# Performance work log

Measured on AMD Instinct MI355X. Metric: run time of the kernel, lower is better.

## Reference

```python
import jax, jax.numpy as jnp
import numpy as np

N = 50000
E = 800000
IN_DIM = 128
HID = 128
OUT = 4
EPS = 1e-5


def setup_inputs() -> dict:
    key = jax.random.key(0)
    ks = jax.random.split(key, 16)
    glorot = lambda k, i, o: jax.random.uniform(k, (i, o), jnp.float32, -1.0, 1.0) * jnp.sqrt(6.0 / (i + o))
    return {
        "x": jax.random.normal(ks[0], (N, IN_DIM), jnp.float32),
        "edge_index": jax.random.randint(ks[1], (2, E), 0, N, jnp.int64),
        # SAGEConv layer 0: lin_l (aggregated neighbors, with bias), lin_r (self, no bias)
        "W_l0": glorot(ks[2], IN_DIM, HID), "b_l0": jnp.zeros((HID,), jnp.float32),
        "W_r0": glorot(ks[3], IN_DIM, HID),
        # SAGEConv layer 1
        "W_l1": glorot(ks[4], HID, HID), "b_l1": jnp.zeros((HID,), jnp.float32),
        "W_r1": glorot(ks[5], HID, HID),
        # LayerNorms
        "g0": jnp.ones((HID,), jnp.float32), "beta0": jnp.zeros((HID,), jnp.float32),
        "g1": jnp.ones((HID,), jnp.float32), "beta1": jnp.zeros((HID,), jnp.float32),
        # head
        "W_h": glorot(ks[6], HID, OUT), "b_h": jnp.zeros((OUT,), jnp.float32),
    }


def _sage_conv(x, src, dst, deg_inv, W_l, b_l, W_r):
    # mean-aggregate source features at destination nodes, then project
    agg = jax.ops.segment_sum(x[src], dst, num_segments=N) * deg_inv  # [N, d]
    return agg @ W_l + b_l + x @ W_r


def _layer_norm(x, g, b):
    mu = jnp.mean(x, axis=-1, keepdims=True)
    var = jnp.mean(jnp.square(x - mu), axis=-1, keepdims=True)
    return (x - mu) * jax.lax.rsqrt(var + EPS) * g + b


def reference(x, edge_index, W_l0, b_l0, W_r0, W_l1, b_l1, W_r1, g0, beta0, g1, beta1, W_h, b_h):
    src, dst = edge_index[0], edge_index[1]
    deg = jax.ops.segment_sum(jnp.ones((E,), jnp.float32), dst, num_segments=N)
    deg_inv = (1.0 / jnp.maximum(deg, 1.0))[:, None]  # mean over empty neighborhood -> 0

    h = _sage_conv(x, src, dst, deg_inv, W_l0, b_l0, W_r0)
    h = jax.nn.relu(_layer_norm(h, g0, beta0))
    h = _sage_conv(h, src, dst, deg_inv, W_l1, b_l1, W_r1)
    h = jax.nn.relu(_layer_norm(h, g1, beta1))
    return h @ W_h + b_h  # [N, 4]
```

## Files before the change

### kernel.cpp

```cpp
#include <hip/hip_runtime.h>

#define NN 50000
#define EE 800000
#define DIM 128
#define KK 256
#define OUTD 4
#define EPSV 1e-5f
#define OTS 132
#define NB 196
#define SLOT 8192
#define ACHUNK 4096
#define NA 196

using short8v = __attribute__((ext_vector_type(8))) short;
using f32x4v  = __attribute__((ext_vector_type(4))) float;

__device__ __forceinline__ unsigned short f2bf(float f) {
    union { float f; unsigned u; } x; x.f = f;
    unsigned r = x.u + 0x7FFF + ((x.u >> 16) & 1);
    return (unsigned short)(r >> 16);
}
__device__ __forceinline__ float bf2f(unsigned short u) {
    union { unsigned u; float f; } x; x.u = ((unsigned)u) << 16;
    return x.f;
}

#define XB_BLK 6250
#define W_BLK  256
__global__ __launch_bounds__(256) void prep_kernel(
    const float* __restrict__ x, ushort* __restrict__ xb,
    const float* __restrict__ Wl0, const float* __restrict__ Wr0,
    const float* __restrict__ Wl1, const float* __restrict__ Wr1,
    ushort* __restrict__ Wt0, ushort* __restrict__ Wt1,
    int* __restrict__ bucketCursor)
{
    int b = blockIdx.x;
    if (b < XB_BLK) {
        int i = b * 256 + threadIdx.x;
        float4 v = ((const float4*)x)[i];
        ushort4 o;
        o.x = f2bf(v.x); o.y = f2bf(v.y); o.z = f2bf(v.z); o.w = f2bf(v.w);
        ((ushort4*)xb)[i] = o;
    } else if (b < XB_BLK + W_BLK) {
        int idx = (b - XB_BLK) * 256 + threadIdx.x;
        int which = idx >> 15;
        int j = (idx >> 8) & 127;
        int k = idx & 255;
        const float* Wl = which ? Wl1 : Wl0;
        const float* Wr = which ? Wr1 : Wr0;
        ushort* Wt = which ? Wt1 : Wt0;
        float v = (k < 128) ? Wl[k * DIM + j] : Wr[(k - 128) * DIM + j];
        Wt[j * KK + k] = f2bf(v);
    } else {
        if (threadIdx.x < NB) bucketCursor[threadIdx.x] = 0;
    }
}

__global__ __launch_bounds__(256) void passA_kernel(
    const int* __restrict__ src, const int* __restrict__ dst,
    int* __restrict__ bucketCursor, unsigned* __restrict__ pairs)
{
    __shared__ int hist[256];
    __shared__ int scanb[256];
    __shared__ int exStart[256];
    __shared__ int cur2[256];
    __shared__ int gBase[256];
    __shared__ unsigned stage[ACHUNK];
    int tid = threadIdx.x;
    int eBase = blockIdx.x * ACHUNK;
    int total = min(ACHUNK, EE - eBase);

    hist[tid] = 0;
    __syncthreads();

    #pragma unroll
    for (int i = 0; i < 16; i++) {
        int idx = i * 256 + tid;
        if (idx < total) {
            int d = dst[eBase + idx];
            atomicAdd(&hist[d >> 8], 1);
        }
    }
    __syncthreads();
    int cntv = hist[tid];
    scanb[tid] = cntv;
    __syncthreads();
    #pragma unroll
    for (int off = 1; off < 256; off <<= 1) {
        int add = (tid >= off) ? scanb[tid - off] : 0;
        __syncthreads();
        scanb[tid] += add;
        __syncthreads();
    }
    int ex = scanb[tid] - cntv;
    exStart[tid] = ex;
    cur2[tid] = ex;
    if (tid < NB) gBase[tid] = (cntv > 0) ? atomicAdd(&bucketCursor[tid], cntv) : 0;
    __syncthreads();

    #pragma unroll
    for (int i = 0; i < 16; i++) {
        int idx = i * 256 + tid;
        if (idx < total) {
            int e = eBase + idx;
            int d = dst[e], s = src[e];
            int bb = d >> 8;
            int sp = atomicAdd(&cur2[bb], 1);
            stage[sp] = ((unsigned)d << 16) | (unsigned)s;
        }
    }
    __syncthreads();

    #pragma unroll
    for (int i = 0; i < 16; i++) {
        int idx = i * 256 + tid;
        if (idx < total) {
            unsigned v = stage[idx];
            int bb = v >> 24;
            int pos = gBase[bb] + (idx - exStart[bb]);
            if (pos < SLOT) pairs[(size_t)bb * SLOT + pos] = v;
        }
    }
}

__global__ __launch_bounds__(256) void passB_kernel(
    const int* __restrict__ bucketCursor,
    const unsigned* __restrict__ pairs,
    int* __restrict__ rowptr, ushort* __restrict__ colS)
{
    __shared__ int bscan[256];
    __shared__ int cw[256];
    __shared__ int pre2[256];
    __shared__ unsigned val_lds[SLOT];
    __shared__ ushort rank_lds[SLOT];
    int tid = threadIdx.x;
    int b = blockIdx.x;

    int c = (tid < NB) ? min(bucketCursor[tid], SLOT) : 0;
    bscan[tid] = c;
    __syncthreads();
    #pragma unroll
    for (int off = 1; off < 256; off <<= 1) {
        int add = (tid >= off) ? bscan[tid - off] : 0;
        __syncthreads();
        bscan[tid] += add;
        __syncthreads();
    }
    int myBase = b ? bscan[b - 1] : 0;
    int count  = bscan[b] - myBase;
    __syncthreads();

    cw[tid] = 0;
    __syncthreads();

    const unsigned* pb = pairs + (size_t)b * SLOT;
    for (int p = tid; p < count; p += 256) {
        unsigned v = pb[p];
        int dl = (v >> 16) & 255;
        int r = atomicAdd(&cw[dl], 1);
        val_lds[p] = v;
        rank_lds[p] = (ushort)r;
    }
    __syncthreads();
    int cnode = cw[tid];
    bscan[tid] = cnode;
    __syncthreads();
    #pragma unroll
    for (int off = 1; off < 256; off <<= 1) {
        int add = (tid >= off) ? bscan[tid - off] : 0;
        __syncthreads();
        bscan[tid] += add;
        __syncthreads();
    }
    int preEx = bscan[tid] - cnode;
    pre2[tid] = preEx;
    int nodeBase = b << 8;
    if (nodeBase + tid < NN) rowptr[nodeBase + tid] = myBase + preEx;
    if (b == NB - 1 && tid == 0) rowptr[NN] = myBase + count;
    __syncthreads();

    for (int p = tid; p < count; p += 256) {
        unsigned v = val_lds[p];
        int dl = (v >> 16) & 255;
        int pos = myBase + pre2[dl] + (int)rank_lds[p];
        colS[pos] = (ushort)(v & 0xFFFF);
    }
}

template <int DO_HEAD>
__global__ __launch_bounds__(256) void sage_fused_kernel(
    const ushort* __restrict__ featG,
    const int* __restrict__ rowptr, const ushort* __restrict__ colS,
    const ushort* __restrict__ WtB,
    const float* __restrict__ bl,
    const float* __restrict__ g, const float* __restrict__ beta,
    const float* __restrict__ Wh, const float* __restrict__ bh,
    void* __restrict__ outp)
{
    __shared__ __align__(16) char smem[32 * OTS * 4];
    __shared__ float mu_s[32], ri_s[32];
    ushort* featB = (ushort*)smem;
    float*  oT    = (float*)smem;
    #define OT(n, k) oT[(n) * OTS + (k)]

    int tid = threadIdx.x;
    int base = blockIdx.x * 32;
    int lane = tid & 63, w = tid >> 6;

    #pragma unroll
    for (int i = 0; i < 2; i++) {
        int idx = tid + i * 256;
        int n = idx >> 4, c = idx & 15;
        int node = base + n;
        short8v xv = {};
        if (node < NN) xv = *(const short8v*)(featG + (size_t)node * DIM + c * 8);
        int kb = (256 + c * 16) ^ ((n & 7) << 4);
        *(short8v*)(featB + n * KK + (kb >> 1)) = xv;
    }

    {
        int lane16 = lane & 15, grp = lane >> 4;
        int rp = 0;
        {
            int ridx = base + w * 8 + lane;
            if (lane < 9) rp = rowptr[min(ridx, NN)];
        }
        for (int i = 0; i < 8; i++) {
            int n = w * 8 + i;
            int beg = __shfl(rp, i, 64);
            int end = __shfl(rp, i + 1, 64);
            int deg = end - beg;
            float a0[8], a1[8];
            #pragma unroll
            for (int c = 0; c < 8; c++) { a0[c] = 0.f; a1[c] = 0.f; }
            int e = beg + grp;
            for (; e + 4 < end; e += 8) {
                int s0 = colS[e], s1 = colS[e + 4];
                short8v v0 = *(const short8v*)(featG + (size_t)s0 * DIM + lane16 * 8);
                short8v v1 = *(const short8v*)(featG + (size_t)s1 * DIM + lane16 * 8);
                #pragma unroll
                for (int c = 0; c < 8; c++) {
                    a0[c] += bf2f((unsigned short)v0[c]);
                    a1[c] += bf2f((unsigned short)v1[c]);
                }
            }
            if (e < end) {
                int s0 = colS[e];
                short8v v0 = *(const short8v*)(featG + (size_t)s0 * DIM + lane16 * 8);
                #pragma unroll
                for (int c = 0; c < 8; c++) a0[c] += bf2f((unsigned short)v0[c]);
            }
            #pragma unroll
            for (int c = 0; c < 8; c++) {
                a0[c] += a1[c];
                a0[c] += __shfl_xor(a0[c], 16, 64);
                a0[c] += __shfl_xor(a0[c], 32, 64);
            }
            if (grp == 0) {
                float di = 1.0f / fmaxf((float)deg, 1.0f);
                short8v o;
                #pragma unroll
                for (int c = 0; c < 8; c++) o[c] = (short)f2bf(a0[c] * di);
                int kb = (lane16 * 16) ^ ((n & 7) << 4);
                *(short8v*)(featB + n * KK + (kb >> 1)) = o;
            }
        }
    }
    __syncthreads();

    int l15 = lane & 15, q = lane >> 4;
    f32x4v acc00 = {}, acc01 = {}, acc10 = {}, acc11 = {};
    const ushort* wbase = WtB + (size_t)(w * 32) * KK;
    int n0 = l15, n1 = 16 + l15;
    int sw = (l15 & 7) << 4;
    #pragma unroll
    for (int ks = 0; ks < 8; ks++) {
        int kbA = ks * 64 + q * 16;
        short8v a0 = *(const short8v*)(featB + n0 * KK + (((kbA) ^ sw) >> 1));
        short8v a1 = *(const short8v*)(featB + n1 * KK + (((kbA) ^ sw) >> 1));
        int koff = ks * 32 + q * 8;
        short8v b0 = *(const short8v*)(wbase + (size_t)l15 * KK + koff);
        short8v b1 = *(const short8v*)(wbase + (size_t)(16 + l15) * KK + koff);
        acc00 = __builtin_amdgcn_mfma_f32_16x16x32_bf16(a0, b0, acc00, 0, 0, 0);
        acc01 = __builtin_amdgcn_mfma_f32_16x16x32_bf16(a0, b1, acc01, 0, 0, 0);
        acc10 = __builtin_amdgcn_mfma_f32_16x16x32_bf16(a1, b0, acc10, 0, 0, 0);
        acc11 = __builtin_amdgcn_mfma_f32_16x16x32_bf16(a1, b1, acc11, 0, 0, 0);
    }
    __syncthreads();

    {
        int c0 = w * 32 + l15, c1 = c0 + 16;
        float bl0v = bl[c0], bl1v = bl[c1];
        #pragma unroll
        for (int r = 0; r < 4; r++) {
            int r0 = q * 4 + r, r1 = 16 + q * 4 + r;
            OT(r0, c0) = acc00[r] + bl0v;
            OT(r0, c1) = acc01[r] + bl1v;
            OT(r1, c0) = acc10[r] + bl0v;
            OT(r1, c1) = acc11[r] + bl1v;
        }
    }
    __syncthreads();

    {
        int n = tid >> 3, l = tid & 7;
        float s = 0.f, s2 = 0.f;
        #pragma unroll
        for (int kk = 0; kk < 16; kk++) {
            float v = OT(n, l * 16 + kk);
            s += v; s2 += v * v;
        }
        #pragma unroll
        for (int off = 4; off; off >>= 1) {
            s  += __shfl_down(s, off, 8);
            s2 += __shfl_down(s2, off, 8);
        }
        if (l == 0) {
            float mu = s * (1.0f / DIM);
            float var = s2 * (1.0f / DIM) - mu * mu;
            mu_s[n] = mu;
            ri_s[n] = rsqrtf(fmaxf(var, 0.f) + EPSV);
        }
    }
    __syncthreads();

    if (!DO_HEAD) {
        ushort* hout = (ushort*)outp;
        #pragma unroll
        for (int i = 0; i < 16; i++) {
            int idx = tid + i * 256;
            int n = idx >> 7, k = idx & 127;
            int node = base + n;
            if (node < NN) {
                float v = (OT(n, k) - mu_s[n]) * ri_s[n] * g[k] + beta[k];
                hout[(size_t)node * DIM + k] = f2bf(fmaxf(v, 0.f));
            }
        }
    } else {
        float* fout = (float*)outp;
        float vals[16];
        #pragma unroll
        for (int i = 0; i < 16; i++) {
            int idx = tid + i * 256;
            int n = idx >> 7, k = idx & 127;
            float v = (OT(n, k) - mu_s[n]) * ri_s[n] * g[k] + beta[k];
            vals[i] = fmaxf(v, 0.f);
        }
        __syncthreads();
        #pragma unroll
        for (int i = 0; i < 16; i++) {
            int idx = tid + i * 256;
            int n = idx >> 7, k = idx & 127;
            OT(n, k) = vals[i];
        }
        __syncthreads();
        if (tid < 128) {
            int n = tid >> 2, o = tid & 3;
            int node = base + n;
            if (node < NN) {
                float s = bh[o];
                for (int k = 0; k < DIM; k++) s += OT(n, k) * Wh[k * OUTD + o];
                fout[(size_t)node * OUTD + o] = s;
            }
        }
    }
    #undef OT
}

extern "C" void kernel_launch(void* const* d_in, const int* in_sizes, int n_in,
                              void* d_out, int out_size, void* d_ws, size_t ws_size,
                              hipStream_t stream)
{
    const float* x    = (const float*)d_in[0];
    const int*   ei   = (const int*)d_in[1];
    const float* Wl0  = (const float*)d_in[2];
    const float* bl0  = (const float*)d_in[3];
    const float* Wr0  = (const float*)d_in[4];
    const float* Wl1  = (const float*)d_in[5];
    const float* bl1  = (const float*)d_in[6];
    const float* Wr1  = (const float*)d_in[7];
    const float* g0   = (const float*)d_in[8];
    const float* be0  = (const float*)d_in[9];
    const float* g1   = (const float*)d_in[10];
    const float* be1  = (const float*)d_in[11];
    const float* Wh   = (const float*)d_in[12];
    const float* bh   = (const float*)d_in[13];
    float* out = (float*)d_out;

    const int* srcI = ei;
    const int* dstI = ei + EE;

    char* p = (char*)d_ws;
    ushort*   xb     = (ushort*)p;    p += (size_t)NN * DIM * 2;
    ushort*   h      = (ushort*)p;    p += (size_t)NN * DIM * 2;
    ushort*   Wt0    = (ushort*)p;    p += DIM * KK * 2;
    ushort*   Wt1    = (ushort*)p;    p += DIM * KK * 2;
    int*      rowptr = (int*)p;       p += 50016 * 4;
    int*      bucketCursor = (int*)p; p += 256 * 4;
    unsigned* pairs  = (unsigned*)p;  p += (size_t)NB * SLOT * 4;
    ushort*   colS   = (ushort*)p;    p += (size_t)EE * 2;

    prep_kernel<<<XB_BLK + W_BLK + 1, 256, 0, stream>>>(
        x, xb, Wl0, Wr0, Wl1, Wr1, Wt0, Wt1, bucketCursor);
    passA_kernel<<<NA, 256, 0, stream>>>(srcI, dstI, bucketCursor, pairs);
    passB_kernel<<<NB, 256, 0, stream>>>(bucketCursor, pairs, rowptr, colS);

    const int blocks = (NN + 31) / 32;
    sage_fused_kernel<0><<<blocks, 256, 0, stream>>>(
        xb, rowptr, colS, Wt0, bl0, g0, be0, nullptr, nullptr, (void*)h);
    sage_fused_kernel<1><<<blocks, 256, 0, stream>>>(
        h, rowptr, colS, Wt1, bl1, g1, be1, Wh, bh, (void*)out);
}
```

Measured before the change: 212.7 us.

## Fuse edge bucketing pass into prep kernel and drop rank buffer in passB

Merges the edge bucketing pass (passA) into the bf16 conversion prep kernel as extra blocks, removing one kernel launch. The bucket cursor is now zeroed with a memset issued before the fused kernel. In passB, the per-edge rank LDS array is removed and ranks are recomputed with a second atomic pass over a reset counter. Every block of the fused kernel now reserves passA's large shared-memory allocation, which may lower occupancy for the conversion blocks. Ordering within a node's edge list may also become nondeterministic.

```diff
diff --git a/kernel.cpp b/kernel.cpp
--- a/kernel.cpp
+++ b/kernel.cpp
@@ -27,22 +27,26 @@
 
 #define XB_BLK 6250
 #define W_BLK  256
-__global__ __launch_bounds__(256) void prep_kernel(
+__global__ __launch_bounds__(256) void prepA_kernel(
     const float* __restrict__ x, ushort* __restrict__ xb,
     const float* __restrict__ Wl0, const float* __restrict__ Wr0,
     const float* __restrict__ Wl1, const float* __restrict__ Wr1,
     ushort* __restrict__ Wt0, ushort* __restrict__ Wt1,
-    int* __restrict__ bucketCursor)
+    const int* __restrict__ src, const int* __restrict__ dst,
+    int* __restrict__ bucketCursor, unsigned* __restrict__ pairs)
 {
     int b = blockIdx.x;
+    int tid = threadIdx.x;
     if (b < XB_BLK) {
-        int i = b * 256 + threadIdx.x;
+        int i = b * 256 + tid;
         float4 v = ((const float4*)x)[i];
         ushort4 o;
         o.x = f2bf(v.x); o.y = f2bf(v.y); o.z = f2bf(v.z); o.w = f2bf(v.w);
         ((ushort4*)xb)[i] = o;
-    } else if (b < XB_BLK + W_BLK) {
-        int idx = (b - XB_BLK) * 256 + threadIdx.x;
+        return;
+    }
+    if (b < XB_BLK + W_BLK) {
+        int idx = (b - XB_BLK) * 256 + tid;
         int which = idx >> 15;
         int j = (idx >> 8) & 127;
         int k = idx & 255;
@@ -51,23 +55,17 @@
         ushort* Wt = which ? Wt1 : Wt0;
         float v = (k < 128) ? Wl[k * DIM + j] : Wr[(k - 128) * DIM + j];
         Wt[j * KK + k] = f2bf(v);
-    } else {
-        if (threadIdx.x < NB) bucketCursor[threadIdx.x] = 0;
-    }
-}
-
-__global__ __launch_bounds__(256) void passA_kernel(
-    const int* __restrict__ src, const int* __restrict__ dst,
-    int* __restrict__ bucketCursor, unsigned* __restrict__ pairs)
-{
+        return;
+    }
+
     __shared__ int hist[256];
     __shared__ int scanb[256];
     __shared__ int exStart[256];
     __shared__ int cur2[256];
     __shared__ int gBase[256];
     __shared__ unsigned stage[ACHUNK];
-    int tid = threadIdx.x;
-    int eBase = blockIdx.x * ACHUNK;
+    int ab = b - XB_BLK - W_BLK;
+    int eBase = ab * ACHUNK;
     int total = min(ACHUNK, EE - eBase);
 
     hist[tid] = 0;
@@ -132,7 +130,6 @@
     __shared__ int cw[256];
     __shared__ int pre2[256];
     __shared__ unsigned val_lds[SLOT];
-    __shared__ ushort rank_lds[SLOT];
     int tid = threadIdx.x;
     int b = blockIdx.x;
 
@@ -156,10 +153,8 @@
     const unsigned* pb = pairs + (size_t)b * SLOT;
     for (int p = tid; p < count; p += 256) {
         unsigned v = pb[p];
-        int dl = (v >> 16) & 255;
-        int r = atomicAdd(&cw[dl], 1);
         val_lds[p] = v;
-        rank_lds[p] = (ushort)r;
+        atomicAdd(&cw[(v >> 16) & 255], 1);
     }
     __syncthreads();
     int cnode = cw[tid];
@@ -177,13 +172,14 @@
     int nodeBase = b << 8;
     if (nodeBase + tid < NN) rowptr[nodeBase + tid] = myBase + preEx;
     if (b == NB - 1 && tid == 0) rowptr[NN] = myBase + count;
+    cw[tid] = 0;
     __syncthreads();
 
     for (int p = tid; p < count; p += 256) {
         unsigned v = val_lds[p];
         int dl = (v >> 16) & 255;
-        int pos = myBase + pre2[dl] + (int)rank_lds[p];
-        colS[pos] = (ushort)(v & 0xFFFF);
+        int r = atomicAdd(&cw[dl], 1);
+        colS[myBase + pre2[dl] + r] = (ushort)(v & 0xFFFF);
     }
 }
 
@@ -400,9 +396,9 @@
     unsigned* pairs  = (unsigned*)p;  p += (size_t)NB * SLOT * 4;
     ushort*   colS   = (ushort*)p;    p += (size_t)EE * 2;
 
-    prep_kernel<<<XB_BLK + W_BLK + 1, 256, 0, stream>>>(
-        x, xb, Wl0, Wr0, Wl1, Wr1, Wt0, Wt1, bucketCursor);
-    passA_kernel<<<NA, 256, 0, stream>>>(srcI, dstI, bucketCursor, pairs);
+    hipMemsetAsync(bucketCursor, 0, 256 * sizeof(int), stream);
+    prepA_kernel<<<XB_BLK + W_BLK + NA, 256, 0, stream>>>(
+        x, xb, Wl0, Wr0, Wl1, Wr1, Wt0, Wt1, srcI, dstI, bucketCursor, pairs);
     passB_kernel<<<NB, 256, 0, stream>>>(bucketCursor, pairs, rowptr, colS);
 
     const int blocks = (NN + 31) / 32;
```

After: 214.8 us. About the same (+1.0%).
